# Kernel tuning notes

Measured on AMD Instinct MI355X. Metric: run time of the kernel, lower is better.

Reference implementation:

```python
import jax, jax.numpy as jnp
import numpy as np

B, T, C_IN, H, K1, NUM_CLASSES = 64, 4096, 64, 96, 128, 109


def conv1d(x, w, b, stride, pad):
    # x: [B, C, T], w: [O, I, K]
    y = jax.lax.conv_general_dilated(x, w, (stride,), [(pad, pad)],
                                     dimension_numbers=('NCH', 'OIH', 'NCH'))
    return y + b[None, :, None]


def bn1d(x, g, b, m, v, eps=1e-5):
    # eval-mode BatchNorm1d over channel dim of [B, C, T]
    scale = g / jnp.sqrt(v + eps)
    return (x - m[None, :, None]) * scale[None, :, None] + b[None, :, None]


def slstm(x, wx, wh, bias):
    # sLSTM block with exponential gating + stabilizer state m (xLSTM paper).
    # x: [B, T, H]; wx, wh: [4H, H] (gate order: z, i, f, o); bias: [4H]
    Bn, Tn, Hn = x.shape
    pre = jnp.einsum('bth,gh->btg', x, wx) + bias  # [B, T, 4H], input part precomputed

    def step(carry, px):
        h, c, n, m = carry
        g = px + h @ wh.T  # [B, 4H]
        zp, ip, fp, op = jnp.split(g, 4, axis=-1)
        z = jnp.tanh(zp)
        o = jax.nn.sigmoid(op)
        m_new = jnp.maximum(fp + m, ip)          # stabilizer
        i = jnp.exp(ip - m_new)
        f = jnp.exp(fp + m - m_new)
        c_new = f * c + i * z
        n_new = f * n + i
        h_new = o * (c_new / jnp.maximum(n_new, 1.0))
        return (h_new, c_new, n_new, m_new), h_new

    z0 = jnp.zeros((Bn, Hn), x.dtype)
    _, ys = jax.lax.scan(step, (z0, z0, z0, z0), pre.transpose(1, 0, 2))
    return ys.transpose(1, 0, 2)  # [B, T, H]


def setup_inputs():
    key = jax.random.key(0)
    ks = jax.random.split(key, 10)

    def rn(k, shape, s=0.05):
        return jax.random.normal(k, shape, jnp.float32) * s

    z = lambda n: jnp.zeros((n,), jnp.float32)
    o = lambda n: jnp.ones((n,), jnp.float32)
    return {
        'x': jax.random.normal(ks[0], (B, T, C_IN), jnp.float32),
        'conv1_w': rn(ks[1], (K1, C_IN, 7)), 'conv1_b': z(K1),
        'bn1_g': o(K1), 'bn1_b': z(K1), 'bn1_m': z(K1), 'bn1_v': o(K1),
        'conv2_w': rn(ks[2], (H, K1, 3)), 'conv2_b': z(H),
        'bn2_g': o(H), 'bn2_b': z(H), 'bn2_m': z(H), 'bn2_v': o(H),
        'res_w': rn(ks[3], (H, K1, 1)), 'res_b': z(H),
        'bnr_g': o(H), 'bnr_b': z(H), 'bnr_m': z(H), 'bnr_v': o(H),
        'slstm_wx': rn(ks[4], (4 * H, H)), 'slstm_wh': rn(ks[5], (4 * H, H)), 'slstm_bias': z(4 * H),
        'fc1_w': rn(ks[6], (128, H)), 'fc1_b': z(128),
        'fc2_w': rn(ks[7], (NUM_CLASSES, 128)), 'fc2_b': z(NUM_CLASSES),
    }


def reference(x, conv1_w, conv1_b, bn1_g, bn1_b, bn1_m, bn1_v,
              conv2_w, conv2_b, bn2_g, bn2_b, bn2_m, bn2_v,
              res_w, res_b, bnr_g, bnr_b, bnr_m, bnr_v,
              slstm_wx, slstm_wh, slstm_bias,
              fc1_w, fc1_b, fc2_w, fc2_b):
    xt = x.transpose(0, 2, 1)  # [B, C_IN, T]
    out = jax.nn.relu(bn1d(conv1d(xt, conv1_w, conv1_b, 1, 3), bn1_g, bn1_b, bn1_m, bn1_v))  # [B, 128, T]
    residual = bn1d(conv1d(out, res_w, res_b, 4, 0), bnr_g, bnr_b, bnr_m, bnr_v)  # [B, H, T//4]
    out = jax.nn.relu(bn1d(conv1d(out, conv2_w, conv2_b, 4, 1), bn2_g, bn2_b, bn2_m, bn2_v)) + residual
    seq = out.transpose(0, 2, 1)  # [B, T//4, H]
    h = slstm(seq, slstm_wx, slstm_wh, slstm_bias)
    pooled = h.mean(axis=1)  # AdaptiveAvgPool1d(1) over time -> [B, H]
    z1 = jax.nn.relu(pooled @ fc1_w.T + fc1_b)
    return z1 @ fc2_w.T + fc2_b  # [B, NUM_CLASSES]
```

## Files before the change

kernel.cpp:

```cpp
#include <hip/hip_runtime.h>
#include <hip/hip_bf16.h>
#include <math.h>

typedef unsigned short u16;
typedef short bf16x8 __attribute__((ext_vector_type(8)));
typedef float f32x4 __attribute__((ext_vector_type(4)));

#define Bz 64
#define Tt 4096
#define Cin 64
#define K1c 128
#define Hh 96
#define T2 1024
#define G4 384
#define NC 109

#define MFMA16(a, b, c) __builtin_amdgcn_mfma_f32_16x16x32_bf16(a, b, c, 0, 0, 0)

__device__ __forceinline__ float bf2f(u16 v) {
  union { unsigned int u; float f; } x; x.u = ((unsigned int)v) << 16; return x.f;
}
__device__ __forceinline__ u16 f2bf(float f) {
  union { unsigned int u; float f; } x; x.f = f;
  unsigned int u = x.u;
  unsigned int r = u + 0x7fff + ((u >> 16) & 1);
  return (u16)(r >> 16);
}

__device__ __forceinline__ float gate_scale(int g) {
  const float L2E = 1.44269504f;
  return (g == 0) ? 2.f * L2E : L2E;
}

__global__ void k_prep(const float* __restrict__ w1, const float* __restrict__ cb1,
                       const float* __restrict__ g1, const float* __restrict__ b1,
                       const float* __restrict__ m1, const float* __restrict__ v1,
                       const float* __restrict__ w2, const float* __restrict__ cb2,
                       const float* __restrict__ g2, const float* __restrict__ b2,
                       const float* __restrict__ m2, const float* __restrict__ v2,
                       const float* __restrict__ wr, const float* __restrict__ cbr,
                       const float* __restrict__ gr, const float* __restrict__ br,
                       const float* __restrict__ mr, const float* __restrict__ vr,
                       const float* __restrict__ wx, const float* __restrict__ sbia,
                       const float* __restrict__ wh,
                       u16* __restrict__ w1b, u16* __restrict__ w2b,
                       u16* __restrict__ wrb, u16* __restrict__ wxb,
                       float* __restrict__ bperm, u16* __restrict__ whb,
                       float* __restrict__ al1, float* __restrict__ be1,
                       float* __restrict__ al2, float* __restrict__ be2,
                       float* __restrict__ alr, float* __restrict__ ber)
{
  int tid = blockIdx.x * blockDim.x + threadIdx.x;
  int nth = gridDim.x * blockDim.x;
  for (int idx = tid; idx < 128 * 448; idx += nth) {
    int o = idx / 448, k = idx % 448;
    int kt = k >> 6, c = k & 63;
    w1b[idx] = f2bf(w1[(o * 64 + c) * 7 + kt]);
  }
  for (int idx = tid; idx < 96 * 384; idx += nth) {
    int o = idx / 384, k = idx % 384;
    int kk = k >> 7, c = k & 127;
    w2b[idx] = f2bf(w2[(o * 128 + c) * 3 + kk]);
  }
  for (int idx = tid; idx < 96 * 128; idx += nth) {
    wrb[idx] = f2bf(wr[idx]);
  }
  for (int idx = tid; idx < 384 * 96; idx += nth) {
    int row = idx / 96, k = idx % 96;
    int ch = row >> 2, g = row & 3;
    wxb[idx] = f2bf(wx[((size_t)(g * 96 + ch)) * 96 + k] * gate_scale(g));
  }
  for (int c = tid; c < 384; c += nth) {
    int ch = c >> 2, g = c & 3;
    bperm[c] = sbia[g * 96 + ch] * gate_scale(g);
  }
  for (int idx = tid; idx < 384 * 96; idx += nth) {
    int row = idx / 96, k = idx % 96;
    int ch = row >> 2, g = row & 3;
    whb[idx] = f2bf(wh[((size_t)(g * 96 + ch)) * 96 + k] * gate_scale(g));
  }
  for (int o = tid; o < 128; o += nth) {
    float a = g1[o] / sqrtf(v1[o] + 1e-5f);
    al1[o] = a; be1[o] = b1[o] + (cb1[o] - m1[o]) * a;
  }
  for (int o = tid; o < 96; o += nth) {
    float a = g2[o] / sqrtf(v2[o] + 1e-5f);
    al2[o] = a; be2[o] = b2[o] + (cb2[o] - m2[o]) * a;
    float ar = gr[o] / sqrtf(vr[o] + 1e-5f);
    alr[o] = ar; ber[o] = br[o] + (cbr[o] - mr[o]) * ar;
  }
}

__launch_bounds__(256, 2)
__global__ void k_conv1(const float* __restrict__ x, const u16* __restrict__ w1b,
                        const float* __restrict__ al1, const float* __restrict__ be1,
                        u16* __restrict__ out1)
{
  __shared__ __align__(16) u16 xs[134 * 72];
  int tid = threadIdx.x;
  int b = blockIdx.y;
  int t0 = blockIdx.x * 128;
  const float* xb = x + (size_t)b * Tt * Cin;

  for (int idx = tid; idx < 134 * 16; idx += 256) {
    int row = idx >> 4, c4 = (idx & 15) << 2;
    int gt = t0 - 3 + row;
    float4 v = make_float4(0.f, 0.f, 0.f, 0.f);
    if (gt >= 0 && gt < Tt) v = *(const float4*)(xb + (size_t)gt * 64 + c4);
    ushort4 s;
    s.x = f2bf(v.x); s.y = f2bf(v.y); s.z = f2bf(v.z); s.w = f2bf(v.w);
    *(ushort4*)(xs + row * 72 + c4) = s;
  }
  __syncthreads();

  int l = tid & 63;
  int wid = tid >> 6;
  int wm = wid >> 1, wn = wid & 1;
  int lr = l & 15, g = l >> 4;

  f32x4 acc[4][4];
#pragma unroll
  for (int i = 0; i < 4; i++)
#pragma unroll
    for (int j = 0; j < 4; j++) acc[i][j] = (f32x4){0.f, 0.f, 0.f, 0.f};

  const u16* wbase = w1b + (size_t)(wn * 64 + lr) * 448;

  for (int s = 0; s < 14; ++s) {
    int kt = s >> 1;
    int cofs = ((s & 1) << 5) + (g << 3);
    const u16* xrow = xs + (wm * 64 + lr + kt) * 72 + cofs;
    bf16x8 a0 = *(const bf16x8*)(xrow);
    bf16x8 a1 = *(const bf16x8*)(xrow + 16 * 72);
    bf16x8 a2 = *(const bf16x8*)(xrow + 32 * 72);
    bf16x8 a3 = *(const bf16x8*)(xrow + 48 * 72);
    int ko = (s << 5) + (g << 3);
    bf16x8 b0 = *(const bf16x8*)(wbase + ko);
    bf16x8 b1 = *(const bf16x8*)(wbase + 16 * 448 + ko);
    bf16x8 b2 = *(const bf16x8*)(wbase + 32 * 448 + ko);
    bf16x8 b3 = *(const bf16x8*)(wbase + 48 * 448 + ko);
    acc[0][0] = MFMA16(a0, b0, acc[0][0]);
    acc[0][1] = MFMA16(a0, b1, acc[0][1]);
    acc[0][2] = MFMA16(a0, b2, acc[0][2]);
    acc[0][3] = MFMA16(a0, b3, acc[0][3]);
    acc[1][0] = MFMA16(a1, b0, acc[1][0]);
    acc[1][1] = MFMA16(a1, b1, acc[1][1]);
    acc[1][2] = MFMA16(a1, b2, acc[1][2]);
    acc[1][3] = MFMA16(a1, b3, acc[1][3]);
    acc[2][0] = MFMA16(a2, b0, acc[2][0]);
    acc[2][1] = MFMA16(a2, b1, acc[2][1]);
    acc[2][2] = MFMA16(a2, b2, acc[2][2]);
    acc[2][3] = MFMA16(a2, b3, acc[2][3]);
    acc[3][0] = MFMA16(a3, b0, acc[3][0]);
    acc[3][1] = MFMA16(a3, b1, acc[3][1]);
    acc[3][2] = MFMA16(a3, b2, acc[3][2]);
    acc[3][3] = MFMA16(a3, b3, acc[3][3]);
  }

  int colb = wn * 64 + lr;
  int rowb = t0 + wm * 64 + (l >> 4) * 4;
#pragma unroll
  for (int nf = 0; nf < 4; nf++) {
    int col = colb + nf * 16;
    float A = al1[col], Bt = be1[col];
#pragma unroll
    for (int mf = 0; mf < 4; mf++) {
      int row = rowb + mf * 16;
#pragma unroll
      for (int r = 0; r < 4; r++) {
        float v = acc[mf][nf][r];
        v = fmaxf(v * A + Bt, 0.f);
        out1[((size_t)b * Tt + row + r) * 128 + col] = f2bf(v);
      }
    }
  }
}

__launch_bounds__(256, 4)
__global__ void k_conv2(const u16* __restrict__ out1, const u16* __restrict__ w2b,
                        const u16* __restrict__ wrb,
                        const float* __restrict__ al2, const float* __restrict__ be2,
                        const float* __restrict__ alr, const float* __restrict__ ber,
                        u16* __restrict__ seqb)
{
  int tid = threadIdx.x;
  int b = blockIdx.y;
  int t20 = blockIdx.x * 64;
  int l = tid & 63;
  int wid = tid >> 6;
  int wm = wid >> 1, wn = wid & 1;
  int lr = l & 15, g = l >> 4;

  f32x4 acc[2][3], accr[2][3];
#pragma unroll
  for (int i = 0; i < 2; i++)
#pragma unroll
    for (int j = 0; j < 3; j++) {
      acc[i][j] = (f32x4){0.f, 0.f, 0.f, 0.f};
      accr[i][j] = (f32x4){0.f, 0.f, 0.f, 0.f};
    }

  const u16* ob = out1 + (size_t)b * Tt * 128;
  int colb = wn * 48 + lr;

#pragma unroll
  for (int f = 0; f < 12; f++) {
    int kk = f >> 2;
    int c = ((f & 3) << 5) + (g << 3);
    bf16x8 a[2];
#pragma unroll
    for (int mf = 0; mf < 2; mf++) {
      int t2 = t20 + wm * 32 + mf * 16 + lr;
      int gt = 4 * t2 + kk - 1;
      if (gt >= 0)
        a[mf] = *(const bf16x8*)(ob + (size_t)gt * 128 + c);
      else
        a[mf] = (bf16x8){0, 0, 0, 0, 0, 0, 0, 0};
    }
#pragma unroll
    for (int nf = 0; nf < 3; nf++) {
      int col = colb + nf * 16;
      bf16x8 bb = *(const bf16x8*)(w2b + (size_t)col * 384 + (f << 5) + (g << 3));
      acc[0][nf] = MFMA16(a[0], bb, acc[0][nf]);
      acc[1][nf] = MFMA16(a[1], bb, acc[1][nf]);
    }
    if (kk == 1) {
#pragma unroll
      for (int nf = 0; nf < 3; nf++) {
        int col = colb + nf * 16;
        bf16x8 br = *(const bf16x8*)(wrb + (size_t)col * 128 + ((f & 3) << 5) + (g << 3));
        accr[0][nf] = MFMA16(a[0], br, accr[0][nf]);
        accr[1][nf] = MFMA16(a[1], br, accr[1][nf]);
      }
    }
  }

  int rowb = t20 + wm * 32 + (l >> 4) * 4;
#pragma unroll
  for (int nf = 0; nf < 3; nf++) {
    int col = colb + nf * 16;
    float A = al2[col], Bt = be2[col];
    float Ar = alr[col], Br = ber[col];
#pragma unroll
    for (int mf = 0; mf < 2; mf++) {
      int row = rowb + mf * 16;
#pragma unroll
      for (int r = 0; r < 4; r++) {
        float v = fmaxf(acc[mf][nf][r] * A + Bt, 0.f) + accr[mf][nf][r] * Ar + Br;
        seqb[((size_t)b * T2 + row + r) * 96 + col] = f2bf(v);
      }
    }
  }
}

__launch_bounds__(512, 1)
__global__ void k_slstm(const u16* __restrict__ seqb, const u16* __restrict__ whb,
                        const u16* __restrict__ wxb, const float* __restrict__ bperm,
                        float* __restrict__ hsum)
{
  __shared__ __align__(16) float pxring[4][384];
  __shared__ __align__(16) u16 hbufB[2][96];
  int tid = threadIdx.x;
  int b = blockIdx.x;
  int w = tid >> 6;
  int l = tid & 63;
  int grp = l >> 4, lr = l & 15;

  if (w < 4) {
    bf16x8 af[6][3];
#pragma unroll
    for (int m = 0; m < 6; m++) {
      const u16* wrow = whb + (size_t)(96 * w + 16 * m + lr) * 96 + grp * 8;
#pragma unroll
      for (int kt = 0; kt < 3; kt++) af[m][kt] = *(const bf16x8*)(wrow + kt * 32);
    }
    bool gl = (lr < 6);
    int ch = 24 * w + 4 * lr + grp;
    float cS = 0.f, nS = 0.f, mS = 0.f, hs = 0.f;
    if (tid < 96) hbufB[0][tid] = 0;
    __syncthreads();

    int p = 0;
    for (int t = 0; t < T2; t++) {
      const float* pxs = &pxring[t & 3][96 * w];
      const u16* hb = hbufB[p] + grp * 8;
      bf16x8 h0 = *(const bf16x8*)(hb);
      bf16x8 h1 = *(const bf16x8*)(hb + 32);
      bf16x8 h2 = *(const bf16x8*)(hb + 64);
      f32x4 acc[6];
#pragma unroll
      for (int m = 0; m < 6; m++) {
        f32x4 pc = *(const f32x4*)(pxs + 16 * m + 4 * grp);
        acc[m] = MFMA16(af[m][0], h0, pc);
        acc[m] = MFMA16(af[m][1], h1, acc[m]);
        acc[m] = MFMA16(af[m][2], h2, acc[m]);
      }
      f32x4 x01 = (lr & 1) ? acc[1] : acc[0];
      f32x4 x23 = (lr & 1) ? acc[3] : acc[2];
      f32x4 x45 = (lr & 1) ? acc[5] : acc[4];
      f32x4 y0 = (lr & 2) ? x23 : x01;
      f32x4 pa = (lr & 4) ? x45 : y0;
      if (gl) {
        float zp = pa[0], ip = pa[1], fp = pa[2], op = pa[3];
        float zc = fminf(fmaxf(zp, -86.f), 86.f);
        float ez = exp2f(zc);
        float z = 1.f - 2.f * __builtin_amdgcn_rcpf(ez + 1.f);
        float oc = fminf(fmaxf(op, -60.f), 60.f);
        float o = __builtin_amdgcn_rcpf(1.f + exp2f(-oc));
        float mn = fmaxf(fp + mS, ip);
        float iv = exp2f(ip - mn);
        float fv = exp2f(fp + mS - mn);
        cS = fv * cS + iv * z;
        nS = fv * nS + iv;
        mS = mn;
        float h = o * cS * __builtin_amdgcn_rcpf(fmaxf(nS, 1.f));
        hs += h;
        hbufB[p ^ 1][ch] = f2bf(h);
      }
      __syncthreads();
      p ^= 1;
    }
    if (gl) hsum[b * 96 + ch] = hs * (1.f / 1024.f);
  } else {
    int pw = w - 4;
    bf16x8 wf[6][3];
#pragma unroll
    for (int m = 0; m < 6; m++) {
      const u16* xrow = wxb + (size_t)(96 * pw + 16 * m + lr) * 96 + grp * 8;
#pragma unroll
      for (int kt = 0; kt < 3; kt++) wf[m][kt] = *(const bf16x8*)(xrow + kt * 32);
    }
    f32x4 bias6[6];
#pragma unroll
    for (int m = 0; m < 6; m++)
      bias6[m] = *(const f32x4*)(bperm + 96 * pw + 16 * m + 4 * grp);

    const u16* sp = seqb + (size_t)b * T2 * 96 + grp * 8;

#pragma unroll
    for (int t0 = 0; t0 < 2; t0++) {
      const u16* s_ = sp + (size_t)t0 * 96;
      bf16x8 s0 = *(const bf16x8*)(s_);
      bf16x8 s1 = *(const bf16x8*)(s_ + 32);
      bf16x8 s2 = *(const bf16x8*)(s_ + 64);
      f32x4 acc[6];
#pragma unroll
      for (int m = 0; m < 6; m++) {
        acc[m] = MFMA16(wf[m][0], s0, bias6[m]);
        acc[m] = MFMA16(wf[m][1], s1, acc[m]);
        acc[m] = MFMA16(wf[m][2], s2, acc[m]);
      }
      if (lr == 0) {
#pragma unroll
        for (int m = 0; m < 6; m++)
          *(f32x4*)(&pxring[t0][96 * pw + 16 * m + 4 * grp]) = acc[m];
      }
    }
    bf16x8 pa0 = *(const bf16x8*)(sp + 2 * 96);
    bf16x8 pa1 = *(const bf16x8*)(sp + 2 * 96 + 32);
    bf16x8 pa2 = *(const bf16x8*)(sp + 2 * 96 + 64);
    bf16x8 pb0 = *(const bf16x8*)(sp + 3 * 96);
    bf16x8 pb1 = *(const bf16x8*)(sp + 3 * 96 + 32);
    bf16x8 pb2 = *(const bf16x8*)(sp + 3 * 96 + 64);
    __syncthreads();

#define PROD_STEP(S0, S1, S2, TT)                                              \
  {                                                                            \
    f32x4 acc_[6];                                                             \
    _Pragma("unroll")                                                          \
    for (int m = 0; m < 6; m++) {                                              \
      acc_[m] = MFMA16(wf[m][0], S0, bias6[m]);                                \
      acc_[m] = MFMA16(wf[m][1], S1, acc_[m]);                                 \
      acc_[m] = MFMA16(wf[m][2], S2, acc_[m]);                                 \
    }                                                                          \
    {                                                                          \
      int tl_ = (TT) + 4 < T2 ? (TT) + 4 : T2 - 1;                             \
      const u16* sp_ = sp + (size_t)tl_ * 96;                                  \
      S0 = *(const bf16x8*)(sp_);                                              \
      S1 = *(const bf16x8*)(sp_ + 32);                                         \
      S2 = *(const bf16x8*)(sp_ + 64);                                         \
    }                                                                          \
    int slot_ = ((TT) + 2) & 3;                                                \
    if (lr == 0) {                                                             \
      _Pragma("unroll")                                                        \
      for (int m = 0; m < 6; m++)                                              \
        *(f32x4*)(&pxring[slot_][96 * pw + 16 * m + 4 * grp]) = acc_[m];       \
    }                                                                          \
    __syncthreads();                                                           \
  }

    for (int t = 0; t < T2; t += 2) {
      PROD_STEP(pa0, pa1, pa2, t);
      PROD_STEP(pb0, pb1, pb2, t + 1);
    }
#undef PROD_STEP
  }
}

__launch_bounds__(128)
__global__ void k_head(const float* __restrict__ hsum, const float* __restrict__ fc1w,
                       const float* __restrict__ fc1b, const float* __restrict__ fc2w,
                       const float* __restrict__ fc2b, float* __restrict__ out)
{
  __shared__ float p[96];
  __shared__ float z1[128];
  int tid = threadIdx.x, b = blockIdx.x;
  if (tid < 96) p[tid] = hsum[b * 96 + tid];
  __syncthreads();
  {
    float a = fc1b[tid];
    const float* wr = fc1w + tid * 96;
    for (int h = 0; h < 96; h++) a += p[h] * wr[h];
    z1[tid] = fmaxf(a, 0.f);
  }
  __syncthreads();
  if (tid < NC) {
    float a = fc2b[tid];
    const float* wr = fc2w + tid * 128;
    for (int j = 0; j < 128; j++) a += z1[j] * wr[j];
    out[b * NC + tid] = a;
  }
}

extern "C" void kernel_launch(void* const* d_in, const int* in_sizes, int n_in,
                              void* d_out, int out_size, void* d_ws, size_t ws_size,
                              hipStream_t stream)
{
  const float* x    = (const float*)d_in[0];
  const float* w1   = (const float*)d_in[1];
  const float* cb1  = (const float*)d_in[2];
  const float* g1   = (const float*)d_in[3];
  const float* b1   = (const float*)d_in[4];
  const float* m1   = (const float*)d_in[5];
  const float* v1   = (const float*)d_in[6];
  const float* w2   = (const float*)d_in[7];
  const float* cb2  = (const float*)d_in[8];
  const float* g2   = (const float*)d_in[9];
  const float* b2   = (const float*)d_in[10];
  const float* m2   = (const float*)d_in[11];
  const float* v2   = (const float*)d_in[12];
  const float* wr   = (const float*)d_in[13];
  const float* cbr  = (const float*)d_in[14];
  const float* gr   = (const float*)d_in[15];
  const float* br   = (const float*)d_in[16];
  const float* mr   = (const float*)d_in[17];
  const float* vr   = (const float*)d_in[18];
  const float* wx   = (const float*)d_in[19];
  const float* wh   = (const float*)d_in[20];
  const float* sbia = (const float*)d_in[21];
  const float* fc1w = (const float*)d_in[22];
  const float* fc1b = (const float*)d_in[23];
  const float* fc2w = (const float*)d_in[24];
  const float* fc2b = (const float*)d_in[25];

  char* ws = (char*)d_ws;
  size_t off = 0;
  auto alloc = [&](size_t bytes) -> void* {
    void* p = (void*)(ws + off);
    off = (off + bytes + 255) & ~((size_t)255);
    return p;
  };
  u16*   out1 = (u16*)  alloc((size_t)Bz * Tt * K1c * 2);
  u16*   seqb = (u16*)  alloc((size_t)Bz * T2 * Hh * 2);
  u16*   w1b  = (u16*)  alloc(448 * 128 * 2);
  u16*   w2b  = (u16*)  alloc(96 * 384 * 2);
  u16*   wrb  = (u16*)  alloc(96 * 128 * 2);
  u16*   wxb  = (u16*)  alloc(384 * 96 * 2);
  float* bperm= (float*)alloc(384 * 4);
  u16*   whb  = (u16*)  alloc(384 * 96 * 2);
  float* al1  = (float*)alloc(128 * 4);
  float* be1  = (float*)alloc(128 * 4);
  float* al2  = (float*)alloc(96 * 4);
  float* be2  = (float*)alloc(96 * 4);
  float* alr  = (float*)alloc(96 * 4);
  float* ber  = (float*)alloc(96 * 4);
  float* hsum = (float*)alloc((size_t)Bz * Hh * 4);
  (void)ws_size; (void)in_sizes; (void)n_in; (void)out_size;

  k_prep<<<dim3(224), dim3(256), 0, stream>>>(
      w1, cb1, g1, b1, m1, v1, w2, cb2, g2, b2, m2, v2,
      wr, cbr, gr, br, mr, vr, wx, sbia, wh,
      w1b, w2b, wrb, wxb, bperm, whb, al1, be1, al2, be2, alr, ber);

  k_conv1<<<dim3(Tt / 128, Bz), dim3(256), 0, stream>>>(x, w1b, al1, be1, out1);

  k_conv2<<<dim3(T2 / 64, Bz), dim3(256), 0, stream>>>(out1, w2b, wrb, al2, be2, alr, ber, seqb);

  k_slstm<<<dim3(Bz), dim3(512), 0, stream>>>(seqb, whb, wxb, bperm, hsum);

  k_head<<<dim3(Bz), dim3(128), 0, stream>>>(hsum, fc1w, fc1b, fc2w, fc2b, (float*)d_out);
}
```

Baseline: 601.6 us.

## Merge producer warps into recurrent warps and batch input projections every 16 steps

The sLSTM kernel drops the four separate producer wavefronts and runs with 256 threads. Each recurrent wave now computes the input projection (Wx·x + bias) for 16 timesteps at once, using all 16 MFMA columns, every 16th step, and stores them in a 32-slot LDS ring. The per-step recurrent MFMA no longer takes the precomputed value as its accumulator; it is added after the gate-row select. The aim is to cut barrier participants and wasted MFMA columns in the sequential loop, at the cost of a heavier step every 16 iterations and more register pressure from holding both weight sets.

```diff
diff --git a/kernel.cpp b/kernel.cpp
--- a/kernel.cpp
+++ b/kernel.cpp
@@ -253,12 +253,12 @@
   }
 }
 
-__launch_bounds__(512, 1)
+__launch_bounds__(256, 1)
 __global__ void k_slstm(const u16* __restrict__ seqb, const u16* __restrict__ whb,
                         const u16* __restrict__ wxb, const float* __restrict__ bperm,
                         float* __restrict__ hsum)
 {
-  __shared__ __align__(16) float pxring[4][384];
+  __shared__ __align__(16) float pxring[32][392];
   __shared__ __align__(16) u16 hbufB[2][96];
   int tid = threadIdx.x;
   int b = blockIdx.x;
@@ -266,135 +266,122 @@
   int l = tid & 63;
   int grp = l >> 4, lr = l & 15;
 
-  if (w < 4) {
-    bf16x8 af[6][3];
+  bf16x8 af[6][3], wf[6][3];
+#pragma unroll
+  for (int m = 0; m < 6; m++) {
+    const u16* wrow = whb + (size_t)(96 * w + 16 * m + lr) * 96 + grp * 8;
+    const u16* xrow = wxb + (size_t)(96 * w + 16 * m + lr) * 96 + grp * 8;
+#pragma unroll
+    for (int kt = 0; kt < 3; kt++) {
+      af[m][kt] = *(const bf16x8*)(wrow + kt * 32);
+      wf[m][kt] = *(const bf16x8*)(xrow + kt * 32);
+    }
+  }
+  f32x4 bias6[6];
+#pragma unroll
+  for (int m = 0; m < 6; m++)
+    bias6[m] = *(const f32x4*)(bperm + 96 * w + 16 * m + 4 * grp);
+
+  bool gl = (lr < 6);
+  int ch = 24 * w + 4 * lr + grp;
+  const u16* sqB = seqb + (size_t)b * T2 * 96 + grp * 8;
+
+  {
+    const u16* sp_ = sqB + (size_t)lr * 96;
+    bf16x8 s0 = *(const bf16x8*)(sp_);
+    bf16x8 s1 = *(const bf16x8*)(sp_ + 32);
+    bf16x8 s2 = *(const bf16x8*)(sp_ + 64);
+    f32x4 pc[6];
 #pragma unroll
     for (int m = 0; m < 6; m++) {
-      const u16* wrow = whb + (size_t)(96 * w + 16 * m + lr) * 96 + grp * 8;
-#pragma unroll
-      for (int kt = 0; kt < 3; kt++) af[m][kt] = *(const bf16x8*)(wrow + kt * 32);
-    }
-    bool gl = (lr < 6);
-    int ch = 24 * w + 4 * lr + grp;
-    float cS = 0.f, nS = 0.f, mS = 0.f, hs = 0.f;
-    if (tid < 96) hbufB[0][tid] = 0;
+      pc[m] = MFMA16(wf[m][0], s0, bias6[m]);
+      pc[m] = MFMA16(wf[m][1], s1, pc[m]);
+      pc[m] = MFMA16(wf[m][2], s2, pc[m]);
+    }
+#pragma unroll
+    for (int m = 0; m < 6; m++)
+      *(f32x4*)(&pxring[lr][96 * w + 16 * m + 4 * grp]) = pc[m];
+  }
+  bf16x8 s0, s1, s2;
+  {
+    int ts = 16 + lr; if (ts > T2 - 1) ts = T2 - 1;
+    const u16* sp_ = sqB + (size_t)ts * 96;
+    s0 = *(const bf16x8*)(sp_);
+    s1 = *(const bf16x8*)(sp_ + 32);
+    s2 = *(const bf16x8*)(sp_ + 64);
+  }
+  if (tid < 96) hbufB[0][tid] = 0;
+  float cS = 0.f, nS = 0.f, mS = 0.f, hs = 0.f;
+  const f32x4 zero4 = {0.f, 0.f, 0.f, 0.f};
+  __syncthreads();
+
+  int p = 0;
+  for (int t = 0; t < T2; t++) {
+    const u16* hb = hbufB[p] + grp * 8;
+    bf16x8 h0 = *(const bf16x8*)(hb);
+    bf16x8 h1 = *(const bf16x8*)(hb + 32);
+    bf16x8 h2 = *(const bf16x8*)(hb + 64);
+    f32x4 pxv = zero4;
+    if (gl) pxv = *(const f32x4*)(&pxring[t & 31][96 * w + 16 * lr + 4 * grp]);
+
+    f32x4 acc[6];
+#pragma unroll
+    for (int m = 0; m < 6; m++) {
+      acc[m] = MFMA16(af[m][0], h0, zero4);
+      acc[m] = MFMA16(af[m][1], h1, acc[m]);
+      acc[m] = MFMA16(af[m][2], h2, acc[m]);
+    }
+
+    bool prod = ((t & 15) == 0) && (t + 16 < T2);
+    f32x4 pacc[6];
+    if (prod) {
+#pragma unroll
+      for (int m = 0; m < 6; m++) {
+        pacc[m] = MFMA16(wf[m][0], s0, bias6[m]);
+        pacc[m] = MFMA16(wf[m][1], s1, pacc[m]);
+        pacc[m] = MFMA16(wf[m][2], s2, pacc[m]);
+      }
+    }
+
+    f32x4 x01 = (lr & 1) ? acc[1] : acc[0];
+    f32x4 x23 = (lr & 1) ? acc[3] : acc[2];
+    f32x4 x45 = (lr & 1) ? acc[5] : acc[4];
+    f32x4 y0 = (lr & 2) ? x23 : x01;
+    f32x4 pa = (lr & 4) ? x45 : y0;
+
+    if (gl) {
+      pa += pxv;
+      float zp = pa[0], ip = pa[1], fp = pa[2], op = pa[3];
+      float zc = fminf(fmaxf(zp, -86.f), 86.f);
+      float ez = exp2f(zc);
+      float z = 1.f - 2.f * __builtin_amdgcn_rcpf(ez + 1.f);
+      float oc = fminf(fmaxf(op, -60.f), 60.f);
+      float o = __builtin_amdgcn_rcpf(1.f + exp2f(-oc));
+      float mn = fmaxf(fp + mS, ip);
+      float iv = exp2f(ip - mn);
+      float fv = exp2f(fp + mS - mn);
+      cS = fv * cS + iv * z;
+      nS = fv * nS + iv;
+      mS = mn;
+      float h = o * cS * __builtin_amdgcn_rcpf(fmaxf(nS, 1.f));
+      hs += h;
+      hbufB[p ^ 1][ch] = f2bf(h);
+    }
+
+    if (prod) {
+#pragma unroll
+      for (int m = 0; m < 6; m++)
+        *(f32x4*)(&pxring[(t + 16 + lr) & 31][96 * w + 16 * m + 4 * grp]) = pacc[m];
+      int ts = t + 32 + lr; if (ts > T2 - 1) ts = T2 - 1;
+      const u16* sp_ = sqB + (size_t)ts * 96;
+      s0 = *(const bf16x8*)(sp_);
+      s1 = *(const bf16x8*)(sp_ + 32);
+      s2 = *(const bf16x8*)(sp_ + 64);
+    }
     __syncthreads();
-
-    int p = 0;
-    for (int t = 0; t < T2; t++) {
-      const float* pxs = &pxring[t & 3][96 * w];
-      const u16* hb = hbufB[p] + grp * 8;
-      bf16x8 h0 = *(const bf16x8*)(hb);
-      bf16x8 h1 = *(const bf16x8*)(hb + 32);
-      bf16x8 h2 = *(const bf16x8*)(hb + 64);
-      f32x4 acc[6];
-#pragma unroll
-      for (int m = 0; m < 6; m++) {
-        f32x4 pc = *(const f32x4*)(pxs + 16 * m + 4 * grp);
-        acc[m] = MFMA16(af[m][0], h0, pc);
-        acc[m] = MFMA16(af[m][1], h1, acc[m]);
-        acc[m] = MFMA16(af[m][2], h2, acc[m]);
-      }
-      f32x4 x01 = (lr & 1) ? acc[1] : acc[0];
-      f32x4 x23 = (lr & 1) ? acc[3] : acc[2];
-      f32x4 x45 = (lr & 1) ? acc[5] : acc[4];
-      f32x4 y0 = (lr & 2) ? x23 : x01;
-      f32x4 pa = (lr & 4) ? x45 : y0;
-      if (gl) {
-        float zp = pa[0], ip = pa[1], fp = pa[2], op = pa[3];
-        float zc = fminf(fmaxf(zp, -86.f), 86.f);
-        float ez = exp2f(zc);
-        float z = 1.f - 2.f * __builtin_amdgcn_rcpf(ez + 1.f);
-        float oc = fminf(fmaxf(op, -60.f), 60.f);
-        float o = __builtin_amdgcn_rcpf(1.f + exp2f(-oc));
-        float mn = fmaxf(fp + mS, ip);
-        float iv = exp2f(ip - mn);
-        float fv = exp2f(fp + mS - mn);
-        cS = fv * cS + iv * z;
-        nS = fv * nS + iv;
-        mS = mn;
-        float h = o * cS * __builtin_amdgcn_rcpf(fmaxf(nS, 1.f));
-        hs += h;
-        hbufB[p ^ 1][ch] = f2bf(h);
-      }
-      __syncthreads();
-      p ^= 1;
-    }
-    if (gl) hsum[b * 96 + ch] = hs * (1.f / 1024.f);
-  } else {
-    int pw = w - 4;
-    bf16x8 wf[6][3];
-#pragma unroll
-    for (int m = 0; m < 6; m++) {
-      const u16* xrow = wxb + (size_t)(96 * pw + 16 * m + lr) * 96 + grp * 8;
-#pragma unroll
-      for (int kt = 0; kt < 3; kt++) wf[m][kt] = *(const bf16x8*)(xrow + kt * 32);
-    }
-    f32x4 bias6[6];
-#pragma unroll
-    for (int m = 0; m < 6; m++)
-      bias6[m] = *(const f32x4*)(bperm + 96 * pw + 16 * m + 4 * grp);
-
-    const u16* sp = seqb + (size_t)b * T2 * 96 + grp * 8;
-
-#pragma unroll
-    for (int t0 = 0; t0 < 2; t0++) {
-      const u16* s_ = sp + (size_t)t0 * 96;
-      bf16x8 s0 = *(const bf16x8*)(s_);
-      bf16x8 s1 = *(const bf16x8*)(s_ + 32);
-      bf16x8 s2 = *(const bf16x8*)(s_ + 64);
-      f32x4 acc[6];
-#pragma unroll
-      for (int m = 0; m < 6; m++) {
-        acc[m] = MFMA16(wf[m][0], s0, bias6[m]);
-        acc[m] = MFMA16(wf[m][1], s1, acc[m]);
-        acc[m] = MFMA16(wf[m][2], s2, acc[m]);
-      }
-      if (lr == 0) {
-#pragma unroll
-        for (int m = 0; m < 6; m++)
-          *(f32x4*)(&pxring[t0][96 * pw + 16 * m + 4 * grp]) = acc[m];
-      }
-    }
-    bf16x8 pa0 = *(const bf16x8*)(sp + 2 * 96);
-    bf16x8 pa1 = *(const bf16x8*)(sp + 2 * 96 + 32);
-    bf16x8 pa2 = *(const bf16x8*)(sp + 2 * 96 + 64);
-    bf16x8 pb0 = *(const bf16x8*)(sp + 3 * 96);
-    bf16x8 pb1 = *(const bf16x8*)(sp + 3 * 96 + 32);
-    bf16x8 pb2 = *(const bf16x8*)(sp + 3 * 96 + 64);
-    __syncthreads();
-
-#define PROD_STEP(S0, S1, S2, TT)                                              \
-  {                                                                            \
-    f32x4 acc_[6];                                                             \
-    _Pragma("unroll")                                                          \
-    for (int m = 0; m < 6; m++) {                                              \
-      acc_[m] = MFMA16(wf[m][0], S0, bias6[m]);                                \
-      acc_[m] = MFMA16(wf[m][1], S1, acc_[m]);                                 \
-      acc_[m] = MFMA16(wf[m][2], S2, acc_[m]);                                 \
-    }                                                                          \
-    {                                                                          \
-      int tl_ = (TT) + 4 < T2 ? (TT) + 4 : T2 - 1;                             \
-      const u16* sp_ = sp + (size_t)tl_ * 96;                                  \
-      S0 = *(const bf16x8*)(sp_);                                              \
-      S1 = *(const bf16x8*)(sp_ + 32);                                         \
-      S2 = *(const bf16x8*)(sp_ + 64);                                         \
-    }                                                                          \
-    int slot_ = ((TT) + 2) & 3;                                                \
-    if (lr == 0) {                                                             \
-      _Pragma("unroll")                                                        \
-      for (int m = 0; m < 6; m++)                                              \
-        *(f32x4*)(&pxring[slot_][96 * pw + 16 * m + 4 * grp]) = acc_[m];       \
-    }                                                                          \
-    __syncthreads();                                                           \
-  }
-
-    for (int t = 0; t < T2; t += 2) {
-      PROD_STEP(pa0, pa1, pa2, t);
-      PROD_STEP(pb0, pb1, pb2, t + 1);
-    }
-#undef PROD_STEP
-  }
+    p ^= 1;
+  }
+  if (gl) hsum[b * 96 + ch] = hs * (1.f / 1024.f);
 }
 
 __launch_bounds__(128)
@@ -486,7 +473,7 @@
 
   k_conv2<<<dim3(T2 / 64, Bz), dim3(256), 0, stream>>>(out1, w2b, wrb, al2, be2, alr, ber, seqb);
 
-  k_slstm<<<dim3(Bz), dim3(512), 0, stream>>>(seqb, whb, wxb, bperm, hsum);
+  k_slstm<<<dim3(Bz), dim3(256), 0, stream>>>(seqb, whb, wxb, bperm, hsum);
 
   k_head<<<dim3(Bz), dim3(128), 0, stream>>>(hsum, fc1w, fc1b, fc2w, fc2b, (float*)d_out);
 }
```

Result: slower. 648.9 us (+7.9%).
